# Optimization experiments

Hardware: AMD Instinct MI355X
Metric: run time of the kernel (lower is better)

## Reference

```python
import jax, jax.numpy as jnp
import numpy as np

B, L, V, D, C, R = 8, 2048, 32000, 512, 64, 64
NBLK = 2           # n_layers - 1
H = 2 * D          # stem hidden dim
STD = 0.02


def _ln(x, w, b):
    m = x.mean(-1, keepdims=True)
    v = ((x - m) ** 2).mean(-1, keepdims=True)
    return (x - m) / jnp.sqrt(v + 1e-5) * w + b


def setup_inputs() -> dict:
    key = jax.random.key(0)
    ks = jax.random.split(key, 16)
    n = lambda k, shp: jax.random.normal(k, shp, dtype=jnp.float32) * STD
    return {
        "token_ids": jax.random.randint(ks[0], (B, L), 0, V),
        "tok_emb": n(ks[1], (V, D)),
        "pos_emb": n(ks[2], (L, D)),
        "stem_ln_w": jnp.ones((NBLK, D), jnp.float32),
        "stem_ln_b": jnp.zeros((NBLK, D), jnp.float32),
        "stem_w1": n(ks[3], (NBLK, D, H)),
        "stem_b1": jnp.zeros((NBLK, H), jnp.float32),
        "stem_w2": n(ks[4], (NBLK, H, D)),
        "stem_b2": jnp.zeros((NBLK, D), jnp.float32),
        "role_ln_w": jnp.ones((D,), jnp.float32),
        "role_ln_b": jnp.zeros((D,), jnp.float32),
        "Wa": n(ks[5], (D, R)),
        "Wb": n(ks[6], (D, R)),
        "Wc": n(ks[7], (D, R)),
        "class_a": n(ks[8], (C, R)),
        "class_b": n(ks[9], (C, R)),
        "class_c": n(ks[10], (C, R)),
        "query_ln_w": jnp.ones((D,), jnp.float32),
        "query_ln_b": jnp.zeros((D,), jnp.float32),
        "Wq": n(ks[11], (D, C)),
        "bq": jnp.zeros((C,), jnp.float32),
    }


def reference(token_ids, tok_emb, pos_emb, stem_ln_w, stem_ln_b, stem_w1,
              stem_b1, stem_w2, stem_b2, role_ln_w, role_ln_b, Wa, Wb, Wc,
              class_a, class_b, class_c, query_ln_w, query_ln_b, Wq, bq):
    seq_len = token_ids.shape[1]
    x = tok_emb[token_ids] + pos_emb[:seq_len][None, :, :]  # [B,L,D]
    for i in range(NBLK):
        h = _ln(x, stem_ln_w[i], stem_ln_b[i])
        h = jax.nn.gelu(h @ stem_w1[i] + stem_b1[i], approximate=False)
        x = x + h @ stem_w2[i] + stem_b2[i]
    prefix = _ln(x[:, :-1], role_ln_w, role_ln_b)  # [B,L-1,D]
    a = jnp.tanh(prefix @ Wa)
    b = jnp.tanh(prefix @ Wb)
    c = jnp.tanh(prefix @ Wc)
    ua = jnp.einsum('blr,cr->blc', a, class_a)  # [B,L-1,C]
    ub = jnp.einsum('blr,cr->blc', b, class_b)
    uc = jnp.einsum('blr,cr->blc', c, class_c)
    # exact ordered-triplet sum  sum_{i<j<k} ua_i * ub_j * uc_k  via exclusive cumsums
    prefA = jnp.cumsum(ua, axis=1) - ua            # sum_{i<j} ua_i
    t = ub * prefA
    prefT = jnp.cumsum(t, axis=1) - t              # sum_{j<k} ub_j * prefA_j
    s = (uc * prefT).sum(axis=1)                   # [B,C]
    Lp = max(seq_len - 1, 1)
    denom = max(Lp * (Lp - 1) * (Lp - 2) / 6.0, 1.0)
    q = _ln(x[:, -1], query_ln_w, query_ln_b)
    return s / denom + q @ Wq + bq
```

## Files before the change

kernel.cpp:

```cpp
#include <hip/hip_runtime.h>

#define NROWS 16384
#define LSEQ  2048
#define NB    8

typedef short v8s __attribute__((ext_vector_type(8)));
typedef float v4f __attribute__((ext_vector_type(4)));

__device__ __forceinline__ unsigned short f2bf(float f) {
    unsigned int u = __float_as_uint(f);
    return (unsigned short)((u + 0x7fffu + ((u >> 16) & 1u)) >> 16);
}

__global__ void transpose_kernel(const float* __restrict__ in, int R, int C,
                                 unsigned short* __restrict__ out, int ldo) {
    __shared__ unsigned short tile[32][33];
    int c0 = blockIdx.x * 32, r0 = blockIdx.y * 32;
    int tx = threadIdx.x, ty = threadIdx.y;
    for (int i = ty; i < 32; i += 8) {
        int r = r0 + i, c = c0 + tx;
        tile[i][tx] = (r < R && c < C) ? f2bf(in[r * C + c]) : (unsigned short)0;
    }
    __syncthreads();
    for (int i = ty; i < 32; i += 8) {
        int c = c0 + i, r = r0 + tx;
        if (r < R && c < C) out[c * ldo + r] = tile[tx][i];
    }
}

__global__ void convert_kernel(const float* __restrict__ in, unsigned short* __restrict__ out, int n) {
    int i = blockIdx.x * 256 + threadIdx.x;
    if (i < n) out[i] = f2bf(in[i]);
}

__global__ __launch_bounds__(256) void embed_ln_kernel(const int* __restrict__ ids,
        const float* __restrict__ tok, const float* __restrict__ pos,
        const float* __restrict__ g, const float* __restrict__ b,
        float* __restrict__ x, unsigned short* __restrict__ hl) {
    int row = blockIdx.x;
    int l = row & (LSEQ - 1);
    int t = threadIdx.x;
    int id = ids[row];
    float a0 = tok[(size_t)id * 512 + t]       + pos[(size_t)l * 512 + t];
    float a1 = tok[(size_t)id * 512 + t + 256] + pos[(size_t)l * 512 + t + 256];
    x[(size_t)row * 512 + t]       = a0;
    x[(size_t)row * 512 + t + 256] = a1;
    float s = a0 + a1, s2 = a0 * a0 + a1 * a1;
    #pragma unroll
    for (int o = 32; o > 0; o >>= 1) { s += __shfl_down(s, o); s2 += __shfl_down(s2, o); }
    __shared__ float ps[4], ps2[4], mv[2];
    int w = t >> 6;
    if ((t & 63) == 0) { ps[w] = s; ps2[w] = s2; }
    __syncthreads();
    if (t == 0) {
        float S = ps[0] + ps[1] + ps[2] + ps[3];
        float S2 = ps2[0] + ps2[1] + ps2[2] + ps2[3];
        float m = S * (1.0f / 512.0f);
        float var = S2 * (1.0f / 512.0f) - m * m;
        mv[0] = m; mv[1] = 1.0f / sqrtf(var + 1e-5f);
    }
    __syncthreads();
    float m = mv[0], r = mv[1];
    hl[(size_t)row * 512 + t]       = f2bf((a0 - m) * r * g[t]       + b[t]);
    hl[(size_t)row * 512 + t + 256] = f2bf((a1 - m) * r * g[t + 256] + b[t + 256]);
}

__global__ __launch_bounds__(256) void ln_kernel(const float* __restrict__ x,
        const float* __restrict__ g, const float* __restrict__ b,
        unsigned short* __restrict__ out) {
    int row = blockIdx.x;
    int t = threadIdx.x;
    const float* xr = x + (size_t)row * 512;
    float a0 = xr[t], a1 = xr[t + 256];
    float s = a0 + a1, s2 = a0 * a0 + a1 * a1;
    #pragma unroll
    for (int o = 32; o > 0; o >>= 1) { s += __shfl_down(s, o); s2 += __shfl_down(s2, o); }
    __shared__ float ps[4], ps2[4], mv[2];
    int w = t >> 6;
    if ((t & 63) == 0) { ps[w] = s; ps2[w] = s2; }
    __syncthreads();
    if (t == 0) {
        float S = ps[0] + ps[1] + ps[2] + ps[3];
        float S2 = ps2[0] + ps2[1] + ps2[2] + ps2[3];
        float m = S * (1.0f / 512.0f);
        float var = S2 * (1.0f / 512.0f) - m * m;
        mv[0] = m; mv[1] = 1.0f / sqrtf(var + 1e-5f);
    }
    __syncthreads();
    float m = mv[0], r = mv[1];
    out[(size_t)row * 512 + t]       = f2bf((a0 - m) * r * g[t]       + b[t]);
    out[(size_t)row * 512 + t + 256] = f2bf((a1 - m) * r * g[t + 256] + b[t + 256]);
}

#define EPI_GELU_BF16  0
#define EPI_RES_F32    1

template <int EPI, int TN>
__global__ __launch_bounds__(256) void gemm_db(
        const unsigned short* __restrict__ A, int lda,
        const unsigned short* __restrict__ BT, int ldb,
        const float* __restrict__ bias,
        void* Cout, int ldc, int K) {
    constexpr int NJ = TN / 32;
    __shared__ unsigned short As[2][128 * 32] __attribute__((aligned(16)));
    __shared__ unsigned short Bs[2][TN * 32] __attribute__((aligned(16)));
    const int t = threadIdx.x;
    const int lane = t & 63, wave = t >> 6;
    const int quad = lane >> 4, l16 = lane & 15;
    const int wm = (wave >> 1) * 64, wn = (wave & 1) * (TN / 2);
    const long tileM = (long)blockIdx.x * 128, tileN = (long)blockIdx.y * TN;

    const int srow = t >> 2, scg = t & 3;
    const int spos = scg ^ ((srow >> 1) & 3);
    const int swz = quad ^ ((l16 >> 1) & 3);
    const int uoff = srow * 32 + spos * 8;

    const unsigned short* gA0 = A + (tileM + srow) * lda + scg * 8;
    const unsigned short* gA1 = gA0 + 64 * (long)lda;
    const unsigned short* gB0 = BT + (tileN + srow) * ldb + scg * 8;
    const unsigned short* gB1 = gB0 + 64 * (long)ldb;

    v4f acc[4][NJ] = {};
    uint4 a0, a1, b0, b1;

    a0 = *(const uint4*)gA0; a1 = *(const uint4*)gA1; gA0 += 32; gA1 += 32;
    b0 = *(const uint4*)gB0; gB0 += 32;
    if (TN == 128) { b1 = *(const uint4*)gB1; gB1 += 32; }
    *(uint4*)&As[0][uoff] = a0;
    *(uint4*)&As[0][uoff + 64 * 32] = a1;
    *(uint4*)&Bs[0][uoff] = b0;
    if (TN == 128) *(uint4*)&Bs[0][uoff + 64 * 32] = b1;

    const int nk = K >> 5;
    for (int kk = 0; kk < nk; ++kk) {
        const int p = kk & 1;
        const bool more = kk + 1 < nk;
        if (more) {
            a0 = *(const uint4*)gA0; a1 = *(const uint4*)gA1; gA0 += 32; gA1 += 32;
            b0 = *(const uint4*)gB0; gB0 += 32;
            if (TN == 128) { b1 = *(const uint4*)gB1; gB1 += 32; }
        }
        __syncthreads();
        v8s af[4], bfr[NJ];
        #pragma unroll
        for (int i = 0; i < 4; ++i) af[i] = *(const v8s*)&As[p][(wm + i * 16 + l16) * 32 + swz * 8];
        #pragma unroll
        for (int j = 0; j < NJ; ++j) bfr[j] = *(const v8s*)&Bs[p][(wn + j * 16 + l16) * 32 + swz * 8];
        #pragma unroll
        for (int i = 0; i < 4; ++i)
            #pragma unroll
            for (int j = 0; j < NJ; ++j)
                acc[i][j] = __builtin_amdgcn_mfma_f32_16x16x32_bf16(af[i], bfr[j], acc[i][j], 0, 0, 0);
        if (more) {
            *(uint4*)&As[1 - p][uoff] = a0;
            *(uint4*)&As[1 - p][uoff + 64 * 32] = a1;
            *(uint4*)&Bs[1 - p][uoff] = b0;
            if (TN == 128) *(uint4*)&Bs[1 - p][uoff + 64 * 32] = b1;
        }
    }

    #pragma unroll
    for (int i = 0; i < 4; ++i) {
        #pragma unroll
        for (int j = 0; j < NJ; ++j) {
            long col = tileN + wn + j * 16 + l16;
            #pragma unroll
            for (int r = 0; r < 4; ++r) {
                long row = tileM + wm + i * 16 + quad * 4 + r;
                float v = acc[i][j][r];
                if (EPI == EPI_GELU_BF16) {
                    v += bias[col];
                    v = 0.5f * v * (1.0f + erff(v * 0.70710678118654752f));
                    ((unsigned short*)Cout)[row * ldc + col] = f2bf(v);
                } else {
                    float* C = (float*)Cout;
                    v += bias[col] + C[row * ldc + col];
                    C[row * ldc + col] = v;
                }
            }
        }
    }
}

__global__ __launch_bounds__(256) void tanh_class_kernel(
        const unsigned short* __restrict__ A,
        const unsigned short* __restrict__ WT,
        const unsigned short* __restrict__ cls,
        float* __restrict__ uu) {
    __shared__ unsigned short As[2][128 * 32] __attribute__((aligned(16)));
    __shared__ unsigned short Bs[2][64 * 32] __attribute__((aligned(16)));
    __shared__ unsigned short P[128 * 72] __attribute__((aligned(16)));
    const int t = threadIdx.x;
    const int lane = t & 63, wave = t >> 6;
    const int quad = lane >> 4, l16 = lane & 15;
    const int wm = (wave >> 1) * 64, wn = (wave & 1) * 32;
    const long tileM = (long)blockIdx.x * 128;
    const int g = blockIdx.y;

    const int srow = t >> 2, scg = t & 3;
    const int spos = scg ^ ((srow >> 1) & 3);
    const int swz = quad ^ ((l16 >> 1) & 3);
    const int uoff = srow * 32 + spos * 8;

    const unsigned short* BT = WT + g * 32768;
    v8s cf[2][2];
    #pragma unroll
    for (int ks = 0; ks < 2; ++ks)
        #pragma unroll
        for (int j = 0; j < 2; ++j)
            cf[ks][j] = *(const v8s*)&cls[g * 4096 + (wn + j * 16 + l16) * 64 + ks * 32 + quad * 8];

    const unsigned short* gA0 = A + (tileM + srow) * 512 + scg * 8;
    const unsigned short* gA1 = gA0 + 64 * 512;
    const unsigned short* gB0 = BT + srow * 512 + scg * 8;

    v4f acc[4][2] = {};
    uint4 a0, a1, b0;
    a0 = *(const uint4*)gA0; a1 = *(const uint4*)gA1; gA0 += 32; gA1 += 32;
    b0 = *(const uint4*)gB0; gB0 += 32;
    *(uint4*)&As[0][uoff] = a0;
    *(uint4*)&As[0][uoff + 64 * 32] = a1;
    *(uint4*)&Bs[0][uoff] = b0;

    for (int kk = 0; kk < 16; ++kk) {
        const int p = kk & 1;
        const bool more = kk < 15;
        if (more) {
            a0 = *(const uint4*)gA0; a1 = *(const uint4*)gA1; gA0 += 32; gA1 += 32;
            b0 = *(const uint4*)gB0; gB0 += 32;
        }
        __syncthreads();
        v8s af[4], bfr[2];
        #pragma unroll
        for (int i = 0; i < 4; ++i) af[i] = *(const v8s*)&As[p][(wm + i * 16 + l16) * 32 + swz * 8];
        #pragma unroll
        for (int j = 0; j < 2; ++j) bfr[j] = *(const v8s*)&Bs[p][(wn + j * 16 + l16) * 32 + swz * 8];
        #pragma unroll
        for (int i = 0; i < 4; ++i)
            #pragma unroll
            for (int j = 0; j < 2; ++j)
                acc[i][j] = __builtin_amdgcn_mfma_f32_16x16x32_bf16(af[i], bfr[j], acc[i][j], 0, 0, 0);
        if (more) {
            *(uint4*)&As[1 - p][uoff] = a0;
            *(uint4*)&As[1 - p][uoff + 64 * 32] = a1;
            *(uint4*)&Bs[1 - p][uoff] = b0;
        }
    }

    #pragma unroll
    for (int i = 0; i < 4; ++i)
        #pragma unroll
        for (int j = 0; j < 2; ++j)
            #pragma unroll
            for (int r = 0; r < 4; ++r)
                P[(wm + i * 16 + quad * 4 + r) * 72 + wn + j * 16 + l16] = f2bf(tanhf(acc[i][j][r]));
    __syncthreads();

    v4f acc2[4][2] = {};
    #pragma unroll
    for (int ks = 0; ks < 2; ++ks) {
        v8s paf[4];
        #pragma unroll
        for (int i = 0; i < 4; ++i)
            paf[i] = *(const v8s*)&P[(wm + i * 16 + l16) * 72 + ks * 32 + quad * 8];
        #pragma unroll
        for (int i = 0; i < 4; ++i)
            #pragma unroll
            for (int j = 0; j < 2; ++j)
                acc2[i][j] = __builtin_amdgcn_mfma_f32_16x16x32_bf16(paf[i], cf[ks][j], acc2[i][j], 0, 0, 0);
    }

    #pragma unroll
    for (int i = 0; i < 4; ++i)
        #pragma unroll
        for (int j = 0; j < 2; ++j) {
            int col = wn + j * 16 + l16;
            #pragma unroll
            for (int r = 0; r < 4; ++r) {
                long row = tileM + wm + i * 16 + quad * 4 + r;
                uu[row * 192 + g * 64 + col] = acc2[i][j][r];
            }
        }
}

__global__ __launch_bounds__(64) void scan_part_kernel(const float* __restrict__ u, float* __restrict__ part) {
    int b = blockIdx.x, seg = blockIdx.y;
    int c = threadIdx.x;
    int l0 = seg * 32;
    int l1 = l0 + 32; if (l1 > 2047) l1 = 2047;
    float sA = 0.f, sB = 0.f, sC = 0.f, T = 0.f, M = 0.f, U = 0.f;
    const float* base = u + ((size_t)b * LSEQ + l0) * 192 + c;
    for (int l = l0; l < l1; ++l) {
        float ua = base[0], ub = base[64], uc = base[128];
        base += 192;
        U += uc * T;
        M += uc * sB;
        T += ub * sA;
        sA += ua; sB += ub; sC += uc;
    }
    float* p = part + ((size_t)(b * 64 + seg)) * 384 + c;
    p[0] = sA; p[64] = sB; p[128] = sC; p[192] = T; p[256] = M; p[320] = U;
}

__global__ __launch_bounds__(64) void scan_combine_kernel(const float* __restrict__ part, float* __restrict__ s) {
    int b = blockIdx.x;
    int c = threadIdx.x;
    const float* p = part + (size_t)b * 64 * 384 + c;
    float A = p[0], B = p[64], Tt = p[192], Mt = p[256], Ut = p[320];
    for (int seg = 1; seg < 64; ++seg) {
        const float* q = p + seg * 384;
        float a2 = q[0], b2 = q[64], c2 = q[128], t2 = q[192], m2 = q[256], u2 = q[320];
        float Un = Ut + u2 + c2 * Tt + A * m2;
        float Tn = Tt + t2 + A * b2;
        float Mn = Mt + m2 + B * c2;
        A += a2; B += b2;
        Ut = Un; Tt = Tn; Mt = Mn;
    }
    s[b * 64 + c] = Ut;
}

__global__ __launch_bounds__(64) void final_kernel(const float* __restrict__ x,
        const float* __restrict__ s,
        const float* __restrict__ qw, const float* __restrict__ qb,
        const float* __restrict__ Wq, const float* __restrict__ bq,
        float* __restrict__ out, float inv_denom) {
    int b = blockIdx.x;
    int c = threadIdx.x;
    __shared__ float q[512];
    __shared__ float mv[2];
    const float* xr = x + ((size_t)b * LSEQ + (LSEQ - 1)) * 512;
    float s1 = 0.f, s2 = 0.f;
    for (int i = c; i < 512; i += 64) { float v = xr[i]; q[i] = v; s1 += v; s2 += v * v; }
    #pragma unroll
    for (int o = 32; o > 0; o >>= 1) { s1 += __shfl_down(s1, o); s2 += __shfl_down(s2, o); }
    if (c == 0) {
        float m = s1 * (1.0f / 512.0f);
        float var = s2 * (1.0f / 512.0f) - m * m;
        mv[0] = m; mv[1] = 1.0f / sqrtf(var + 1e-5f);
    }
    __syncthreads();
    float m = mv[0], r = mv[1];
    for (int i = c; i < 512; i += 64) q[i] = (q[i] - m) * r * qw[i] + qb[i];
    __syncthreads();
    float acc = 0.f;
    for (int d = 0; d < 512; ++d) acc += q[d] * Wq[d * 64 + c];
    out[b * 64 + c] = s[b * 64 + c] * inv_denom + acc + bq[c];
}

extern "C" void kernel_launch(void* const* d_in, const int* in_sizes, int n_in,
                              void* d_out, int out_size, void* d_ws, size_t ws_size,
                              hipStream_t stream) {
    const int*   token_ids   = (const int*)d_in[0];
    const float* tok_emb     = (const float*)d_in[1];
    const float* pos_emb     = (const float*)d_in[2];
    const float* stem_ln_w   = (const float*)d_in[3];
    const float* stem_ln_b   = (const float*)d_in[4];
    const float* stem_w1     = (const float*)d_in[5];
    const float* stem_b1     = (const float*)d_in[6];
    const float* stem_w2     = (const float*)d_in[7];
    const float* stem_b2     = (const float*)d_in[8];
    const float* role_ln_w   = (const float*)d_in[9];
    const float* role_ln_b   = (const float*)d_in[10];
    const float* Wa          = (const float*)d_in[11];
    const float* Wb          = (const float*)d_in[12];
    const float* Wc          = (const float*)d_in[13];
    const float* class_a     = (const float*)d_in[14];
    const float* class_b     = (const float*)d_in[15];
    const float* class_c     = (const float*)d_in[16];
    const float* query_ln_w  = (const float*)d_in[17];
    const float* query_ln_b  = (const float*)d_in[18];
    const float* Wq          = (const float*)d_in[19];
    const float* bq          = (const float*)d_in[20];
    float* out = (float*)d_out;

    char* wsb = (char*)d_ws;
    float* x             = (float*)(wsb);
    unsigned short* hl   = (unsigned short*)(wsb + 33554432);
    unsigned short* Hb   = (unsigned short*)(wsb + 50331648);
    float* uu            = (float*)(wsb + 58720256);
    float* part          = (float*)(wsb + 71303168);
    float* svec          = (float*)(wsb + 72089600);
    unsigned short* w1T  = (unsigned short*)(wsb + 83886080);
    unsigned short* w2T  = (unsigned short*)(wsb + 85983232);
    unsigned short* wabcT= (unsigned short*)(wsb + 88080384);
    unsigned short* clsb = (unsigned short*)(wsb + 88276992);

    dim3 tb(32, 8);
    transpose_kernel<<<dim3(32, 16), tb, 0, stream>>>(stem_w1,          512, 1024, w1T,          512);
    transpose_kernel<<<dim3(32, 16), tb, 0, stream>>>(stem_w1 + 524288, 512, 1024, w1T + 524288, 512);
    transpose_kernel<<<dim3(16, 32), tb, 0, stream>>>(stem_w2,          1024, 512, w2T,          1024);
    transpose_kernel<<<dim3(16, 32), tb, 0, stream>>>(stem_w2 + 524288, 1024, 512, w2T + 524288, 1024);
    transpose_kernel<<<dim3(2, 16),  tb, 0, stream>>>(Wa, 512, 64, wabcT,         512);
    transpose_kernel<<<dim3(2, 16),  tb, 0, stream>>>(Wb, 512, 64, wabcT + 32768, 512);
    transpose_kernel<<<dim3(2, 16),  tb, 0, stream>>>(Wc, 512, 64, wabcT + 65536, 512);
    convert_kernel<<<16, 256, 0, stream>>>(class_a, clsb,        4096);
    convert_kernel<<<16, 256, 0, stream>>>(class_b, clsb + 4096, 4096);
    convert_kernel<<<16, 256, 0, stream>>>(class_c, clsb + 8192, 4096);

    embed_ln_kernel<<<NROWS, 256, 0, stream>>>(token_ids, tok_emb, pos_emb,
                                               stem_ln_w, stem_ln_b, x, hl);

    for (int i = 0; i < 2; ++i) {
        if (i > 0)
            ln_kernel<<<NROWS, 256, 0, stream>>>(x, stem_ln_w + 512, stem_ln_b + 512, hl);
        gemm_db<EPI_GELU_BF16, 128><<<dim3(128, 8), 256, 0, stream>>>(
            hl, 512, w1T + i * 524288, 512, stem_b1 + i * 1024, Hb, 1024, 512);
        gemm_db<EPI_RES_F32, 64><<<dim3(128, 8), 256, 0, stream>>>(
            Hb, 1024, w2T + i * 524288, 1024, stem_b2 + i * 512, x, 512, 1024);
    }

    ln_kernel<<<NROWS, 256, 0, stream>>>(x, role_ln_w, role_ln_b, hl);

    tanh_class_kernel<<<dim3(128, 3), 256, 0, stream>>>(hl, wabcT, clsb, uu);

    scan_part_kernel<<<dim3(NB, 64), 64, 0, stream>>>(uu, part);
    scan_combine_kernel<<<NB, 64, 0, stream>>>(part, svec);

    float inv_denom = (float)(6.0 / (2047.0 * 2046.0 * 2045.0));
    final_kernel<<<NB, 64, 0, stream>>>(x, svec, query_ln_w, query_ln_b, Wq, bq, out, inv_denom);
}
```

Measured before the change: 400.7 us.

## Store residual stream and class projections in bf16, merge prep kernels, fast gelu/tanh

Stores the residual stream x and the class projection buffer in bf16 instead of fp32, which halves their memory traffic in the LN, GEMM epilogue, scan and final kernels. It merges the ten weight transpose/convert launches into one prep kernel. It replaces erff and tanhf with polynomial/exp approximations and vectorises the LN loads and stores. The GEMM drops the swizzled double-buffered LDS for a single padded buffer with two barriers per k-step. Keeping the residual in bf16 across layers loses accuracy, and the single buffer may reduce overlap.

```diff
diff --git a/kernel.cpp b/kernel.cpp
--- a/kernel.cpp
+++ b/kernel.cpp
@@ -11,40 +11,81 @@
     unsigned int u = __float_as_uint(f);
     return (unsigned short)((u + 0x7fffu + ((u >> 16) & 1u)) >> 16);
 }
-
-__global__ void transpose_kernel(const float* __restrict__ in, int R, int C,
-                                 unsigned short* __restrict__ out, int ldo) {
-    __shared__ unsigned short tile[32][33];
-    int c0 = blockIdx.x * 32, r0 = blockIdx.y * 32;
+__device__ __forceinline__ float bf2f(unsigned short u) {
+    return __uint_as_float(((unsigned int)u) << 16);
+}
+
+__device__ __forceinline__ float fast_gelu(float v) {
+    float z = fabsf(v) * 0.70710678118654752f;
+    float t = __builtin_amdgcn_rcpf(1.0f + 0.3275911f * z);
+    float poly = t * (0.254829592f + t * (-0.284496736f + t * (1.421413741f +
+                 t * (-1.453152027f + t * 1.061405429f))));
+    float erfz = 1.0f - poly * __expf(-z * z);
+    float er = copysignf(erfz, v);
+    return 0.5f * v * (1.0f + er);
+}
+__device__ __forceinline__ float fast_tanh(float y) {
+    float e = __expf(2.0f * y);
+    return (e - 1.0f) * __builtin_amdgcn_rcpf(e + 1.0f);
+}
+
+__global__ __launch_bounds__(256) void prep_kernel(
+        const float* __restrict__ w1, const float* __restrict__ w2,
+        const float* __restrict__ wa, const float* __restrict__ wb, const float* __restrict__ wc,
+        const float* __restrict__ ca, const float* __restrict__ cb, const float* __restrict__ cc,
+        unsigned short* __restrict__ w1T, unsigned short* __restrict__ w2T,
+        unsigned short* __restrict__ wabcT, unsigned short* __restrict__ clsb) {
+    int id = blockIdx.x;
     int tx = threadIdx.x, ty = threadIdx.y;
-    for (int i = ty; i < 32; i += 8) {
-        int r = r0 + i, c = c0 + tx;
-        tile[i][tx] = (r < R && c < C) ? f2bf(in[r * C + c]) : (unsigned short)0;
-    }
-    __syncthreads();
-    for (int i = ty; i < 32; i += 8) {
-        int c = c0 + i, r = r0 + tx;
-        if (r < R && c < C) out[c * ldo + r] = tile[tx][i];
-    }
-}
-
-__global__ void convert_kernel(const float* __restrict__ in, unsigned short* __restrict__ out, int n) {
-    int i = blockIdx.x * 256 + threadIdx.x;
-    if (i < n) out[i] = f2bf(in[i]);
+    if (id < 2144) {
+        const float* in; unsigned short* out; int R, C, bx, by, ldo;
+        if (id < 1024) {
+            int l = id >> 9, r = id & 511;
+            in = w1 + l * 524288; out = w1T + l * 524288;
+            R = 512; C = 1024; bx = r & 31; by = r >> 5; ldo = 512;
+        } else if (id < 2048) {
+            int l = (id - 1024) >> 9, r = (id - 1024) & 511;
+            in = w2 + l * 524288; out = w2T + l * 524288;
+            R = 1024; C = 512; bx = r & 15; by = r >> 4; ldo = 1024;
+        } else {
+            int g = (id - 2048) >> 5, r = (id - 2048) & 31;
+            in = (g == 0) ? wa : (g == 1) ? wb : wc;
+            out = wabcT + g * 32768;
+            R = 512; C = 64; bx = r & 1; by = r >> 1; ldo = 512;
+        }
+        __shared__ unsigned short tile[32][33];
+        int c0 = bx * 32, r0 = by * 32;
+        for (int i = ty; i < 32; i += 8) {
+            int r = r0 + i, c = c0 + tx;
+            tile[i][tx] = (r < R && c < C) ? f2bf(in[(size_t)r * C + c]) : (unsigned short)0;
+        }
+        __syncthreads();
+        for (int i = ty; i < 32; i += 8) {
+            int c = c0 + i, r = r0 + tx;
+            if (r < R && c < C) out[(size_t)c * ldo + r] = tile[tx][i];
+        }
+    } else {
+        int g = id - 2144;
+        const float* src = (g == 0) ? ca : (g == 1) ? cb : cc;
+        unsigned short* dst = clsb + g * 4096;
+        int tid = ty * 32 + tx;
+        for (int i = tid; i < 4096; i += 256) dst[i] = f2bf(src[i]);
+    }
 }
 
 __global__ __launch_bounds__(256) void embed_ln_kernel(const int* __restrict__ ids,
         const float* __restrict__ tok, const float* __restrict__ pos,
         const float* __restrict__ g, const float* __restrict__ b,
-        float* __restrict__ x, unsigned short* __restrict__ hl) {
+        unsigned short* __restrict__ x, unsigned short* __restrict__ hl) {
     int row = blockIdx.x;
     int l = row & (LSEQ - 1);
     int t = threadIdx.x;
     int id = ids[row];
-    float a0 = tok[(size_t)id * 512 + t]       + pos[(size_t)l * 512 + t];
-    float a1 = tok[(size_t)id * 512 + t + 256] + pos[(size_t)l * 512 + t + 256];
-    x[(size_t)row * 512 + t]       = a0;
-    x[(size_t)row * 512 + t + 256] = a1;
+    float2 tv = *(const float2*)(tok + (size_t)id * 512 + 2 * t);
+    float2 pv = *(const float2*)(pos + (size_t)l * 512 + 2 * t);
+    float a0 = tv.x + pv.x, a1 = tv.y + pv.y;
+    unsigned int xp = (unsigned int)f2bf(a0) | ((unsigned int)f2bf(a1) << 16);
+    *(unsigned int*)(x + (size_t)row * 512 + 2 * t) = xp;
     float s = a0 + a1, s2 = a0 * a0 + a1 * a1;
     #pragma unroll
     for (int o = 32; o > 0; o >>= 1) { s += __shfl_down(s, o); s2 += __shfl_down(s2, o); }
@@ -61,17 +102,18 @@
     }
     __syncthreads();
     float m = mv[0], r = mv[1];
-    hl[(size_t)row * 512 + t]       = f2bf((a0 - m) * r * g[t]       + b[t]);
-    hl[(size_t)row * 512 + t + 256] = f2bf((a1 - m) * r * g[t + 256] + b[t + 256]);
-}
-
-__global__ __launch_bounds__(256) void ln_kernel(const float* __restrict__ x,
+    unsigned int hp = (unsigned int)f2bf((a0 - m) * r * g[2 * t] + b[2 * t])
+                    | ((unsigned int)f2bf((a1 - m) * r * g[2 * t + 1] + b[2 * t + 1]) << 16);
+    *(unsigned int*)(hl + (size_t)row * 512 + 2 * t) = hp;
+}
+
+__global__ __launch_bounds__(256) void ln_kernel(const unsigned short* __restrict__ x,
         const float* __restrict__ g, const float* __restrict__ b,
         unsigned short* __restrict__ out) {
     int row = blockIdx.x;
     int t = threadIdx.x;
-    const float* xr = x + (size_t)row * 512;
-    float a0 = xr[t], a1 = xr[t + 256];
+    unsigned int xp = *(const unsigned int*)(x + (size_t)row * 512 + 2 * t);
+    float a0 = bf2f((unsigned short)(xp & 0xffff)), a1 = bf2f((unsigned short)(xp >> 16));
     float s = a0 + a1, s2 = a0 * a0 + a1 * a1;
     #pragma unroll
     for (int o = 32; o > 0; o >>= 1) { s += __shfl_down(s, o); s2 += __shfl_down(s2, o); }
@@ -88,36 +130,34 @@
     }
     __syncthreads();
     float m = mv[0], r = mv[1];
-    out[(size_t)row * 512 + t]       = f2bf((a0 - m) * r * g[t]       + b[t]);
-    out[(size_t)row * 512 + t + 256] = f2bf((a1 - m) * r * g[t + 256] + b[t + 256]);
+    unsigned int hp = (unsigned int)f2bf((a0 - m) * r * g[2 * t] + b[2 * t])
+                    | ((unsigned int)f2bf((a1 - m) * r * g[2 * t + 1] + b[2 * t + 1]) << 16);
+    *(unsigned int*)(out + (size_t)row * 512 + 2 * t) = hp;
 }
 
 #define EPI_GELU_BF16  0
-#define EPI_RES_F32    1
+#define EPI_RES_BF16   1
 
 template <int EPI, int TN>
-__global__ __launch_bounds__(256) void gemm_db(
+__global__ __launch_bounds__(256) void gemm_r2(
         const unsigned short* __restrict__ A, int lda,
         const unsigned short* __restrict__ BT, int ldb,
         const float* __restrict__ bias,
-        void* Cout, int ldc, int K) {
+        const unsigned short* __restrict__ xres,
+        unsigned short* __restrict__ Cout, int ldc, int K) {
     constexpr int NJ = TN / 32;
-    __shared__ unsigned short As[2][128 * 32] __attribute__((aligned(16)));
-    __shared__ unsigned short Bs[2][TN * 32] __attribute__((aligned(16)));
+    __shared__ unsigned short As[128][40] __attribute__((aligned(16)));
+    __shared__ unsigned short Bs[TN][40] __attribute__((aligned(16)));
     const int t = threadIdx.x;
     const int lane = t & 63, wave = t >> 6;
     const int quad = lane >> 4, l16 = lane & 15;
     const int wm = (wave >> 1) * 64, wn = (wave & 1) * (TN / 2);
     const long tileM = (long)blockIdx.x * 128, tileN = (long)blockIdx.y * TN;
-
-    const int srow = t >> 2, scg = t & 3;
-    const int spos = scg ^ ((srow >> 1) & 3);
-    const int swz = quad ^ ((l16 >> 1) & 3);
-    const int uoff = srow * 32 + spos * 8;
-
-    const unsigned short* gA0 = A + (tileM + srow) * lda + scg * 8;
+    const int arow = t >> 2, acol = (t & 3) * 8;
+
+    const unsigned short* gA0 = A + (tileM + arow) * lda + acol;
     const unsigned short* gA1 = gA0 + 64 * (long)lda;
-    const unsigned short* gB0 = BT + (tileN + srow) * ldb + scg * 8;
+    const unsigned short* gB0 = BT + (tileN + arow) * ldb + acol;
     const unsigned short* gB1 = gB0 + 64 * (long)ldb;
 
     v4f acc[4][NJ] = {};
@@ -126,36 +166,36 @@
     a0 = *(const uint4*)gA0; a1 = *(const uint4*)gA1; gA0 += 32; gA1 += 32;
     b0 = *(const uint4*)gB0; gB0 += 32;
     if (TN == 128) { b1 = *(const uint4*)gB1; gB1 += 32; }
-    *(uint4*)&As[0][uoff] = a0;
-    *(uint4*)&As[0][uoff + 64 * 32] = a1;
-    *(uint4*)&Bs[0][uoff] = b0;
-    if (TN == 128) *(uint4*)&Bs[0][uoff + 64 * 32] = b1;
+    *(uint4*)&As[arow][acol] = a0;
+    *(uint4*)&As[arow + 64][acol] = a1;
+    *(uint4*)&Bs[arow][acol] = b0;
+    if (TN == 128) *(uint4*)&Bs[arow + 64][acol] = b1;
 
     const int nk = K >> 5;
     for (int kk = 0; kk < nk; ++kk) {
-        const int p = kk & 1;
+        __syncthreads();
         const bool more = kk + 1 < nk;
         if (more) {
             a0 = *(const uint4*)gA0; a1 = *(const uint4*)gA1; gA0 += 32; gA1 += 32;
             b0 = *(const uint4*)gB0; gB0 += 32;
             if (TN == 128) { b1 = *(const uint4*)gB1; gB1 += 32; }
         }
-        __syncthreads();
         v8s af[4], bfr[NJ];
         #pragma unroll
-        for (int i = 0; i < 4; ++i) af[i] = *(const v8s*)&As[p][(wm + i * 16 + l16) * 32 + swz * 8];
-        #pragma unroll
-        for (int j = 0; j < NJ; ++j) bfr[j] = *(const v8s*)&Bs[p][(wn + j * 16 + l16) * 32 + swz * 8];
+        for (int i = 0; i < 4; ++i) af[i] = *(const v8s*)&As[wm + i * 16 + l16][quad * 8];
+        #pragma unroll
+        for (int j = 0; j < NJ; ++j) bfr[j] = *(const v8s*)&Bs[wn + j * 16 + l16][quad * 8];
         #pragma unroll
         for (int i = 0; i < 4; ++i)
             #pragma unroll
             for (int j = 0; j < NJ; ++j)
                 acc[i][j] = __builtin_amdgcn_mfma_f32_16x16x32_bf16(af[i], bfr[j], acc[i][j], 0, 0, 0);
+        __syncthreads();
         if (more) {
-            *(uint4*)&As[1 - p][uoff] = a0;
-            *(uint4*)&As[1 - p][uoff + 64 * 32] = a1;
-            *(uint4*)&Bs[1 - p][uoff] = b0;
-            if (TN == 128) *(uint4*)&Bs[1 - p][uoff + 64 * 32] = b1;
+            *(uint4*)&As[arow][acol] = a0;
+            *(uint4*)&As[arow + 64][acol] = a1;
+            *(uint4*)&Bs[arow][acol] = b0;
+            if (TN == 128) *(uint4*)&Bs[arow + 64][acol] = b1;
         }
     }
 
@@ -169,13 +209,11 @@
                 long row = tileM + wm + i * 16 + quad * 4 + r;
                 float v = acc[i][j][r];
                 if (EPI == EPI_GELU_BF16) {
-                    v += bias[col];
-                    v = 0.5f * v * (1.0f + erff(v * 0.70710678118654752f));
-                    ((unsigned short*)Cout)[row * ldc + col] = f2bf(v);
+                    v = fast_gelu(v + bias[col]);
+                    Cout[row * ldc + col] = f2bf(v);
                 } else {
-                    float* C = (float*)Cout;
-                    v += bias[col] + C[row * ldc + col];
-                    C[row * ldc + col] = v;
+                    v += bias[col] + bf2f(xres[row * ldc + col]);
+                    Cout[row * ldc + col] = f2bf(v);
                 }
             }
         }
@@ -186,7 +224,7 @@
         const unsigned short* __restrict__ A,
         const unsigned short* __restrict__ WT,
         const unsigned short* __restrict__ cls,
-        float* __restrict__ uu) {
+        unsigned short* __restrict__ uu) {
     __shared__ unsigned short As[2][128 * 32] __attribute__((aligned(16)));
     __shared__ unsigned short Bs[2][64 * 32] __attribute__((aligned(16)));
     __shared__ unsigned short P[128 * 72] __attribute__((aligned(16)));
@@ -253,7 +291,7 @@
         for (int j = 0; j < 2; ++j)
             #pragma unroll
             for (int r = 0; r < 4; ++r)
-                P[(wm + i * 16 + quad * 4 + r) * 72 + wn + j * 16 + l16] = f2bf(tanhf(acc[i][j][r]));
+                P[(wm + i * 16 + quad * 4 + r) * 72 + wn + j * 16 + l16] = f2bf(fast_tanh(acc[i][j][r]));
     __syncthreads();
 
     v4f acc2[4][2] = {};
@@ -278,20 +316,21 @@
             #pragma unroll
             for (int r = 0; r < 4; ++r) {
                 long row = tileM + wm + i * 16 + quad * 4 + r;
-                uu[row * 192 + g * 64 + col] = acc2[i][j][r];
+                uu[row * 192 + g * 64 + col] = f2bf(acc2[i][j][r]);
             }
         }
 }
 
-__global__ __launch_bounds__(64) void scan_part_kernel(const float* __restrict__ u, float* __restrict__ part) {
+__global__ __launch_bounds__(64) void scan_part_kernel(const unsigned short* __restrict__ u,
+                                                       float* __restrict__ part) {
     int b = blockIdx.x, seg = blockIdx.y;
     int c = threadIdx.x;
     int l0 = seg * 32;
     int l1 = l0 + 32; if (l1 > 2047) l1 = 2047;
     float sA = 0.f, sB = 0.f, sC = 0.f, T = 0.f, M = 0.f, U = 0.f;
-    const float* base = u + ((size_t)b * LSEQ + l0) * 192 + c;
+    const unsigned short* base = u + ((size_t)b * LSEQ + l0) * 192 + c;
     for (int l = l0; l < l1; ++l) {
-        float ua = base[0], ub = base[64], uc = base[128];
+        float ua = bf2f(base[0]), ub = bf2f(base[64]), uc = bf2f(base[128]);
         base += 192;
         U += uc * T;
         M += uc * sB;
@@ -302,7 +341,8 @@
     p[0] = sA; p[64] = sB; p[128] = sC; p[192] = T; p[256] = M; p[320] = U;
 }
 
-__global__ __launch_bounds__(64) void scan_combine_kernel(const float* __restrict__ part, float* __restrict__ s) {
+__global__ __launch_bounds__(64) void scan_combine_kernel(const float* __restrict__ part,
+                                                          float* __restrict__ s) {
     int b = blockIdx.x;
     int c = threadIdx.x;
     const float* p = part + (size_t)b * 64 * 384 + c;
@@ -319,7 +359,7 @@
     s[b * 64 + c] = Ut;
 }
 
-__global__ __launch_bounds__(64) void final_kernel(const float* __restrict__ x,
+__global__ __launch_bounds__(64) void final_kernel(const unsigned short* __restrict__ x,
         const float* __restrict__ s,
         const float* __restrict__ qw, const float* __restrict__ qb,
         const float* __restrict__ Wq, const float* __restrict__ bq,
@@ -328,9 +368,9 @@
     int c = threadIdx.x;
     __shared__ float q[512];
     __shared__ float mv[2];
-    const float* xr = x + ((size_t)b * LSEQ + (LSEQ - 1)) * 512;
+    const unsigned short* xr = x + ((size_t)b * LSEQ + (LSEQ - 1)) * 512;
     float s1 = 0.f, s2 = 0.f;
-    for (int i = c; i < 512; i += 64) { float v = xr[i]; q[i] = v; s1 += v; s2 += v * v; }
+    for (int i = c; i < 512; i += 64) { float v = bf2f(xr[i]); q[i] = v; s1 += v; s2 += v * v; }
     #pragma unroll
     for (int o = 32; o > 0; o >>= 1) { s1 += __shfl_down(s1, o); s2 += __shfl_down(s2, o); }
     if (c == 0) {
@@ -374,28 +414,19 @@
     float* out = (float*)d_out;
 
     char* wsb = (char*)d_ws;
-    float* x             = (float*)(wsb);
-    unsigned short* hl   = (unsigned short*)(wsb + 33554432);
-    unsigned short* Hb   = (unsigned short*)(wsb + 50331648);
-    float* uu            = (float*)(wsb + 58720256);
-    float* part          = (float*)(wsb + 71303168);
-    float* svec          = (float*)(wsb + 72089600);
-    unsigned short* w1T  = (unsigned short*)(wsb + 83886080);
-    unsigned short* w2T  = (unsigned short*)(wsb + 85983232);
-    unsigned short* wabcT= (unsigned short*)(wsb + 88080384);
-    unsigned short* clsb = (unsigned short*)(wsb + 88276992);
-
-    dim3 tb(32, 8);
-    transpose_kernel<<<dim3(32, 16), tb, 0, stream>>>(stem_w1,          512, 1024, w1T,          512);
-    transpose_kernel<<<dim3(32, 16), tb, 0, stream>>>(stem_w1 + 524288, 512, 1024, w1T + 524288, 512);
-    transpose_kernel<<<dim3(16, 32), tb, 0, stream>>>(stem_w2,          1024, 512, w2T,          1024);
-    transpose_kernel<<<dim3(16, 32), tb, 0, stream>>>(stem_w2 + 524288, 1024, 512, w2T + 524288, 1024);
-    transpose_kernel<<<dim3(2, 16),  tb, 0, stream>>>(Wa, 512, 64, wabcT,         512);
-    transpose_kernel<<<dim3(2, 16),  tb, 0, stream>>>(Wb, 512, 64, wabcT + 32768, 512);
-    transpose_kernel<<<dim3(2, 16),  tb, 0, stream>>>(Wc, 512, 64, wabcT + 65536, 512);
-    convert_kernel<<<16, 256, 0, stream>>>(class_a, clsb,        4096);
-    convert_kernel<<<16, 256, 0, stream>>>(class_b, clsb + 4096, 4096);
-    convert_kernel<<<16, 256, 0, stream>>>(class_c, clsb + 8192, 4096);
+    unsigned short* x    = (unsigned short*)(wsb);
+    unsigned short* hl   = (unsigned short*)(wsb + 16777216);
+    unsigned short* Hb   = (unsigned short*)(wsb + 33554432);
+    unsigned short* uu   = (unsigned short*)(wsb + 67108864);
+    float* part          = (float*)(wsb + 73400320);
+    float* svec          = (float*)(wsb + 74186752);
+    unsigned short* w1T  = (unsigned short*)(wsb + 74188800);
+    unsigned short* w2T  = (unsigned short*)(wsb + 76285952);
+    unsigned short* wabcT= (unsigned short*)(wsb + 78383104);
+    unsigned short* clsb = (unsigned short*)(wsb + 78579712);
+
+    prep_kernel<<<2147, dim3(32, 8), 0, stream>>>(stem_w1, stem_w2, Wa, Wb, Wc,
+        class_a, class_b, class_c, w1T, w2T, wabcT, clsb);
 
     embed_ln_kernel<<<NROWS, 256, 0, stream>>>(token_ids, tok_emb, pos_emb,
                                                stem_ln_w, stem_ln_b, x, hl);
@@ -403,10 +434,10 @@
     for (int i = 0; i < 2; ++i) {
         if (i > 0)
             ln_kernel<<<NROWS, 256, 0, stream>>>(x, stem_ln_w + 512, stem_ln_b + 512, hl);
-        gemm_db<EPI_GELU_BF16, 128><<<dim3(128, 8), 256, 0, stream>>>(
-            hl, 512, w1T + i * 524288, 512, stem_b1 + i * 1024, Hb, 1024, 512);
-        gemm_db<EPI_RES_F32, 64><<<dim3(128, 8), 256, 0, stream>>>(
-            Hb, 1024, w2T + i * 524288, 1024, stem_b2 + i * 512, x, 512, 1024);
+        gemm_r2<EPI_GELU_BF16, 128><<<dim3(128, 8), 256, 0, stream>>>(
+            hl, 512, w1T + i * 524288, 512, stem_b1 + i * 1024, nullptr, Hb, 1024, 512);
+        gemm_r2<EPI_RES_BF16, 64><<<dim3(128, 8), 256, 0, stream>>>(
+            Hb, 1024, w2T + i * 524288, 1024, stem_b2 + i * 512, x, x, 512, 1024);
     }
 
     ln_kernel<<<NROWS, 256, 0, stream>>>(x, role_ln_w, role_ln_b, hl);
```

Result: faster. 354.8 us (-11.5%).
